# Kernel tuning notes

Hardware: AMD Instinct MI355X
Metric: run time of the kernel (lower is better)

## Reference

```python
import jax, jax.numpy as jnp
import numpy as np

B, M, P = 128, 35, 224  # batch, num Zernike modes, pupil_size
SIGN_PENALTY = 10.0
RECON_WEIGHT = 0.4
DEFOCUS_RAD = 1.0
EPS = 1e-8


def setup_inputs() -> dict:
    key = jax.random.key(0)
    k1, k2, k3, k4 = jax.random.split(key, 4)
    pred = jax.random.normal(k1, (B, M), dtype=jnp.float32)
    target = jax.random.normal(k2, (B, M), dtype=jnp.float32)
    input_psfs = jax.random.uniform(k3, (B, 2, P, P), dtype=jnp.float32)
    zernike_basis = jax.random.normal(k4, (M, P, P), dtype=jnp.float32)
    pupil_mask = jnp.ones((P, P), dtype=jnp.float32)
    return {
        "pred": pred,
        "target": target,
        "input_psfs": input_psfs,
        "zernike_basis": zernike_basis,
        "pupil_mask": pupil_mask,
    }


def _psf_from_phase(phase, pupil_mask):
    # phase: [B,P,P] real; pupil: masked complex field
    pupil = pupil_mask[None, :, :] * jnp.exp(1j * phase)
    field = jnp.fft.fftshift(jnp.fft.fft2(pupil), axes=(-2, -1))
    psf = field.real ** 2 + field.imag ** 2  # |FFT|^2
    psf = psf / (psf.sum(axis=(-2, -1), keepdims=True) + EPS)
    return psf


def reference(pred, target, input_psfs, zernike_basis, pupil_mask):
    # --- sign-weighted MSE on Zernike coefficients ---
    base = (pred - target) ** 2
    sign_match = jnp.sign(pred) * jnp.sign(target)
    weight = jnp.where(sign_match < 0, SIGN_PENALTY, 1.0)
    z_loss = jnp.mean(base * weight)

    # --- batched differentiable PSF reconstruction loss ---
    phase = jnp.einsum('bm,mhw->bhw', pred, zernike_basis)
    phase = phase * pupil_mask[None, :, :]

    sim_if = _psf_from_phase(phase, pupil_mask)  # in-focus

    lin = jnp.linspace(-1.0, 1.0, P, dtype=jnp.float32)
    y, x = jnp.meshgrid(lin, lin, indexing='ij')
    r2 = x ** 2 + y ** 2
    defocus_phase = DEFOCUS_RAD * (2.0 * r2 - 1.0)  # [P,P]
    sim_podf = _psf_from_phase(phase + defocus_phase[None, :, :], pupil_mask)

    # per-sample F.mse_loss then mean over batch == mean over the batched arrays
    recon_loss = (jnp.mean((sim_if - input_psfs[:, 0]) ** 2)
                  + jnp.mean((sim_podf - input_psfs[:, 1]) ** 2))

    return z_loss + RECON_WEIGHT * recon_loss
```

## Files before the change

### kernel.cpp

```cpp
#include <hip/hip_runtime.h>
#include <math.h>

#define BB 128
#define MM 35
#define PSZ 224
#define PP (PSZ*PSZ)
#define SIGN_PENALTY 10.0f
#define RECON_WEIGHT 0.4f
#define DEFOCUS_RAD 1.0f
#define EPS_F 1e-8f
#define INV2PI 0.15915494309189535f


#define WS_PHASE_OFF    2048
#define WS_T_OFF        (WS_PHASE_OFF + BB*PP)
#define N_PARTIALS      (14*BB*2)
#define S1 233
#define S2 20

static constexpr float W16R[16] = {
    1.0f, 0.9238795325f, 0.7071067812f, 0.3826834324f, 0.0f,
    -0.3826834324f, -0.7071067812f, -0.9238795325f, -1.0f,
    -0.9238795325f, -0.7071067812f, -0.3826834324f, 0.0f,
    0.3826834324f, 0.7071067812f, 0.9238795325f};
static constexpr float W16I[16] = {
    0.0f, -0.3826834324f, -0.7071067812f, -0.9238795325f, -1.0f,
    -0.9238795325f, -0.7071067812f, -0.3826834324f, 0.0f,
    0.3826834324f, 0.7071067812f, 0.9238795325f, 1.0f,
    0.9238795325f, 0.7071067812f, 0.3826834324f};
static constexpr float W7R[7] = {
    1.0f, 0.6234898019f, -0.2225209340f, -0.9009688679f,
    -0.9009688679f, -0.2225209340f, 0.6234898019f};
static constexpr float W7I[7] = {
    0.0f, -0.7818314825f, -0.9749279122f, -0.4338837391f,
    0.4338837391f, 0.9749279122f, 0.7818314825f};
static constexpr float W14R[7] = {
    1.0f, 0.9009688679f, 0.6234898019f, 0.2225209340f, -0.2225209340f,
    -0.6234898019f, -0.9009688679f};
static constexpr float W14I[7] = {
    0.0f, -0.4338837391f, -0.7818314825f, -0.9749279122f, -0.9749279122f,
    -0.7818314825f, -0.4338837391f};

__device__ __forceinline__ float lincoord(int i) {
    return -1.0f + 2.0f * (float)i / (float)(PSZ - 1);
}
__device__ __forceinline__ void fast_sincos(float x, float* s, float* c) {
    float rv = x * INV2PI;
    rv -= floorf(rv);
    *s = __builtin_amdgcn_sinf(rv);
    *c = __builtin_amdgcn_cosf(rv);
}
__device__ __forceinline__ float2 wexp_neg(float frac) {
    float rv = -frac;
    rv -= floorf(rv);
    return make_float2(__builtin_amdgcn_cosf(rv), __builtin_amdgcn_sinf(rv));
}
__device__ __forceinline__ unsigned pack_bf2(float a, float b) {
    unsigned r;
    asm("v_cvt_pk_bf16_f32 %0, %1, %2" : "=v"(r) : "v"(a), "v"(b));
    return r;
}
__device__ __forceinline__ float2 unpack_bf2(unsigned v) {
    return make_float2(__uint_as_float(v << 16), __uint_as_float(v & 0xffff0000u));
}
__device__ __forceinline__ float2 cmul(float2 a, float2 b) {
    return make_float2(fmaf(a.x, b.x, -a.y * b.y), fmaf(a.x, b.y, a.y * b.x));
}
__device__ __forceinline__ float2 cmulc(float2 a, float wr, float wi) {
    return make_float2(fmaf(a.x, wr, -a.y * wi), fmaf(a.x, wi, a.y * wr));
}
__device__ __forceinline__ float2 cadd(float2 a, float2 b) {
    return make_float2(a.x + b.x, a.y + b.y);
}
__device__ __forceinline__ float2 csub(float2 a, float2 b) {
    return make_float2(a.x - b.x, a.y - b.y);
}
__device__ __forceinline__ void cfma(float& acc, float c, float v) {
    if (c == 0.f) return;
    if (c == 1.f)  { acc += v; return; }
    if (c == -1.f) { acc -= v; return; }
    acc = fmaf(c, v, acc);
}

__device__ __forceinline__ void dft8_sym(const float2* u, float2* X) {
    float2 a1 = cadd(u[1], u[7]), b1 = csub(u[1], u[7]);
    float2 a2 = cadd(u[2], u[6]), b2 = csub(u[2], u[6]);
    float2 a3 = cadd(u[3], u[5]), b3 = csub(u[3], u[5]);
    float2 s04 = cadd(u[0], u[4]), d04 = csub(u[0], u[4]);
    X[0] = cadd(cadd(s04, a1), cadd(a2, a3));
    X[4] = cadd(csub(s04, a1), csub(a2, a3));
    {
        float2 p = csub(s04, a2);
        float2 q = csub(b1, b3);
        X[2] = make_float2(p.x + q.y, p.y - q.x);
        X[6] = make_float2(p.x - q.y, p.y + q.x);
    }
#pragma unroll
    for (int m = 1; m <= 3; m += 2) {
        float Px = d04.x, Py = d04.y, Qx = 0.f, Qy = 0.f;
#pragma unroll
        for (int n = 1; n <= 3; n++) {
            const float cR = W16R[(2 * n * m) & 15], cI = W16I[(2 * n * m) & 15];
            const float2 a = (n == 1) ? a1 : (n == 2) ? a2 : a3;
            const float2 b = (n == 1) ? b1 : (n == 2) ? b2 : b3;
            cfma(Px, cR, a.x); cfma(Py, cR, a.y);
            cfma(Qx, cI, b.x); cfma(Qy, cI, b.y);
        }
        X[m]     = make_float2(Px - Qy, Py + Qx);
        X[8 - m] = make_float2(Px + Qy, Py - Qx);
    }
}

__device__ __forceinline__ void dft7_sym(const float2* x, float2* X) {
    float2 a1 = cadd(x[1], x[6]), b1 = csub(x[1], x[6]);
    float2 a2 = cadd(x[2], x[5]), b2 = csub(x[2], x[5]);
    float2 a3 = cadd(x[3], x[4]), b3 = csub(x[3], x[4]);
    X[0] = cadd(cadd(x[0], a1), cadd(a2, a3));
#pragma unroll
    for (int k = 1; k <= 3; k++) {
        float Px = x[0].x, Py = x[0].y, Qx = 0.f, Qy = 0.f;
#pragma unroll
        for (int n = 1; n <= 3; n++) {
            const float cR = W7R[(n * k) % 7], cI = W7I[(n * k) % 7];
            const float2 a = (n == 1) ? a1 : (n == 2) ? a2 : a3;
            const float2 b = (n == 1) ? b1 : (n == 2) ? b2 : b3;
            cfma(Px, cR, a.x); cfma(Py, cR, a.y);
            cfma(Qx, cI, b.x); cfma(Qy, cI, b.y);
        }
        X[k]     = make_float2(Px - Qy, Py + Qx);
        X[7 - k] = make_float2(Px + Qy, Py - Qx);
    }
}

__device__ __forceinline__ void inner16_core(const float2* xin,
                                             unsigned* __restrict__ xbuf,
                                             int base, int mul, int n1) {
    float2 u[8], v[8];
#pragma unroll
    for (int n = 0; n < 8; n++) {
        u[n] = cadd(xin[n], xin[n + 8]);
        float2 w = csub(xin[n], xin[n + 8]);
        v[n] = (n == 0) ? w : cmulc(w, W16R[n], W16I[n]);
    }
    float2 u1w = wexp_neg((float)n1 * (1.0f / 224.0f));
    float2 u2w = wexp_neg((float)n1 * (1.0f / 112.0f));
    {
        float2 Xe[8];
        dft8_sym(u, Xe);
        float2 cur = make_float2(1.f, 0.f);
#pragma unroll
        for (int m = 0; m < 8; m++) {
            float2 z = (m == 0) ? Xe[0] : cmul(Xe[m], cur);
            xbuf[base + (14 * (2 * m)) * mul] = pack_bf2(z.x, z.y);
            cur = cmul(cur, u2w);
        }
    }
    {
        float2 Xo[8];
        dft8_sym(v, Xo);
        float2 cur = u1w;
#pragma unroll
        for (int m = 0; m < 8; m++) {
            float2 z = cmul(Xo[m], cur);
            xbuf[base + (14 * (2 * m + 1)) * mul] = pack_bf2(z.x, z.y);
            cur = cmul(cur, u2w);
        }
    }
}

__global__ __launch_bounds__(256) void k_phase(const float* __restrict__ pred,
                                               const float* __restrict__ target,
                                               const float* __restrict__ zern,
                                               const float* __restrict__ mask,
                                               float* __restrict__ phase,
                                               float* __restrict__ ws) {
    __shared__ float pl[32 * MM];
    __shared__ float red[256];
    int t = threadIdx.x;
    if (blockIdx.x == 196) {
        int y = blockIdx.y;
        float s = 0.f;
        if (y == 0) {
            for (int i = t; i < BB * MM; i += 256) {
                float p = pred[i], tg = target[i];
                float dd = p - tg;
                float w = (p * tg < 0.f) ? SIGN_PENALTY : 1.f;
                s = fmaf(dd * dd, w, s);
            }
        } else {
            const int F4 = PP / 4;
            int st = (y - 1) * 4182;
            int en = (y == 3) ? F4 : st + 4182;
            const float4* m4 = (const float4*)mask;
            for (int i = st + t; i < en; i += 256) {
                float4 v = m4[i];
                s = fmaf(v.x, v.x, s); s = fmaf(v.y, v.y, s);
                s = fmaf(v.z, v.z, s); s = fmaf(v.w, v.w, s);
            }
        }
        red[t] = s;
        __syncthreads();
        for (int st = 128; st > 0; st >>= 1) {
            if (t < st) red[t] += red[t + st];
            __syncthreads();
        }
        if (t == 0) {
            if (y == 0) ws[1] = red[0] / (float)(BB * MM);
            else        ws[1 + y] = red[0];
        }
        return;
    }
    int bg = blockIdx.y;
    for (int i = t; i < 32 * MM; i += 256) {
        int j = i / MM, m = i % MM;
        pl[i] = pred[(bg * 32 + j) * MM + m];
    }
    __syncthreads();
    int pix = blockIdx.x * 256 + t;
    float acc[32];
#pragma unroll
    for (int j = 0; j < 32; j++) acc[j] = 0.f;
    for (int m = 0; m < MM; m++) {
        float z = zern[m * PP + pix];
#pragma unroll
        for (int j = 0; j < 32; j++) acc[j] = fmaf(pl[j * MM + m], z, acc[j]);
    }
    float mk = mask[pix];
#pragma unroll
    for (int j = 0; j < 32; j++) phase[(size_t)(bg * 32 + j) * PP + pix] = acc[j] * mk;
}

__global__ __launch_bounds__(256, 5) void k_stage1(const float* __restrict__ phase,
                                                   const float* __restrict__ mask,
                                                   unsigned* __restrict__ T) {
    __shared__ unsigned xs0[16 * S1];
    __shared__ unsigned xs1[16 * S1];
    int h0 = blockIdx.x * 16;
    int b = blockIdx.y;
    int t = threadIdx.x;

    if (t < 224) {
        int r = t / 14, n1 = t - (t / 14) * 14;
        const float* phr = phase + (size_t)b * PP + (size_t)(h0 + r) * PSZ;
        const float* mkr = mask + (size_t)(h0 + r) * PSZ;
        float vy = lincoord(h0 + r);
        float vy2m1 = DEFOCUS_RAD * (2.f * vy * vy - 1.f);
        float2 x0[16];
        unsigned x1p[16];
#pragma unroll
        for (int n = 0; n < 16; n++) {
            int col = n1 + 14 * n;
            float ph = phr[col];
            float mk = mkr[col];
            float sn, cs;
            fast_sincos(ph, &sn, &cs);
            float vx = lincoord(col);
            float df = fmaf(2.f * DEFOCUS_RAD, vx * vx, vy2m1);
            float sd, cd;
            fast_sincos(df, &sd, &cd);
            float c0 = mk * cs, s0 = mk * sn;
            x0[n] = make_float2(c0, s0);
            x1p[n] = pack_bf2(fmaf(c0, cd, -s0 * sd), fmaf(s0, cd, c0 * sd));
        }
        inner16_core(x0, xs0, r * S1 + n1, 1, n1);
        float2 x1[16];
#pragma unroll
        for (int n = 0; n < 16; n++) x1[n] = unpack_bf2(x1p[n]);
        inner16_core(x1, xs1, r * S1 + n1, 1, n1);
    }
    __syncthreads();

    {
        int r = t >> 4, k2 = t & 15;
#pragma unroll
        for (int dd = 0; dd < 2; dd++) {
            const unsigned* xr = (dd ? xs1 : xs0) + r * S1 + k2 * 14;
            int img = dd * BB + b;
            unsigned* Tt = T + (((size_t)img * 14) * PSZ + (h0 + r)) * 16 + k2;
            float2 e[7], E[7], O[7];
#pragma unroll
            for (int n = 0; n < 7; n++) e[n] = unpack_bf2(xr[2 * n]);
            dft7_sym(e, E);
#pragma unroll
            for (int n = 0; n < 7; n++) e[n] = unpack_bf2(xr[2 * n + 1]);
            dft7_sym(e, O);
#pragma unroll
            for (int k1 = 0; k1 < 7; k1++) {
                float2 op = (k1 == 0) ? O[0] : cmulc(O[k1], W14R[k1], W14I[k1]);
                float2 s = cadd(E[k1], op), q = csub(E[k1], op);
                Tt[(size_t)k1 * (PSZ * 16)]       = pack_bf2(s.x, s.y);
                Tt[(size_t)(k1 + 7) * (PSZ * 16)] = pack_bf2(q.x, q.y);
            }
        }
    }
}

__global__ __launch_bounds__(256, 6) void k_stage2(const unsigned* __restrict__ T,
                                                   const float* __restrict__ psfs,
                                                   const float* __restrict__ ws,
                                                   float* __restrict__ partials) {
    __shared__ unsigned xs[224 * S2];
    __shared__ float red[4];
    int tile = blockIdx.x, b = blockIdx.y, d = blockIdx.z;
    int img = d * BB + b;
    int t = threadIdx.x;
    int k2o = t >> 4, c = t & 15;

    const unsigned* Tb = T + ((size_t)img * 14 + tile) * (PSZ * 16);
    const float* inp = psfs + ((size_t)b * 2 + d) * PP;
    int scol = 16 * ((tile + 7) % 14) + c;
    float pf[14];
#pragma unroll
    for (int j = 0; j < 7; j++) {
        pf[j]     = inp[(size_t)(112 + 16 * j + k2o) * PSZ + scol];
        pf[j + 7] = inp[(size_t)(16 * j + k2o) * PSZ + scol];
    }

    if (t < 224) {
        int n1 = t >> 4, cc = t & 15;
        float2 x[16];
#pragma unroll
        for (int n = 0; n < 16; n++)
            x[n] = unpack_bf2(Tb[224 * n + t]);
        inner16_core(x, xs, n1 * S2 + cc, S2, n1);
    }
    __syncthreads();

    float m2 = ws[2] + ws[3] + ws[4];
    float inv_denom = 1.f / (m2 * (float)PP + EPS_F);

    float lsum = 0.f;
    {
        float2 e[7], E[7], O[7];
#pragma unroll
        for (int n = 0; n < 7; n++) e[n] = unpack_bf2(xs[(k2o * 14 + 2 * n) * S2 + c]);
        dft7_sym(e, E);
#pragma unroll
        for (int n = 0; n < 7; n++) e[n] = unpack_bf2(xs[(k2o * 14 + 2 * n + 1) * S2 + c]);
        dft7_sym(e, O);
#pragma unroll
        for (int k1 = 0; k1 < 7; k1++) {
            float2 op = (k1 == 0) ? O[0] : cmulc(O[k1], W14R[k1], W14I[k1]);
            float2 s = cadd(E[k1], op), q = csub(E[k1], op);
            float ds = fmaf(s.x, s.x, s.y * s.y) * inv_denom - pf[k1];
            float dq = fmaf(q.x, q.x, q.y * q.y) * inv_denom - pf[k1 + 7];
            lsum = fmaf(ds, ds, lsum);
            lsum = fmaf(dq, dq, lsum);
        }
    }
#pragma unroll
    for (int off = 32; off > 0; off >>= 1)
        lsum += __shfl_down(lsum, off, 64);
    if ((t & 63) == 0) red[t >> 6] = lsum;
    __syncthreads();
    if (t == 0)
        partials[(blockIdx.z * BB + blockIdx.y) * 14 + blockIdx.x] =
            red[0] + red[1] + red[2] + red[3];
}

__global__ void k_final(const float* __restrict__ ws,
                        const float* __restrict__ partials,
                        float* __restrict__ out) {
    __shared__ float red[256];
    float s = 0.f;
    for (int i = threadIdx.x; i < N_PARTIALS; i += 256) s += partials[i];
    red[threadIdx.x] = s;
    __syncthreads();
    for (int st = 128; st > 0; st >>= 1) {
        if (threadIdx.x < st) red[threadIdx.x] += red[threadIdx.x + st];
        __syncthreads();
    }
    if (threadIdx.x == 0) {
        float recon = red[0] / (float)((size_t)BB * PP);
        out[0] = ws[1] + RECON_WEIGHT * recon;
    }
}

extern "C" void kernel_launch(void* const* d_in, const int* in_sizes, int n_in,
                              void* d_out, int out_size, void* d_ws, size_t ws_size,
                              hipStream_t stream) {
    const float* pred   = (const float*)d_in[0];
    const float* target = (const float*)d_in[1];
    const float* psfs   = (const float*)d_in[2];
    const float* zern   = (const float*)d_in[3];
    const float* mask   = (const float*)d_in[4];

    float*    ws       = (float*)d_ws;
    float*    phase    = ws + WS_PHASE_OFF;
    float*    partials = ws + WS_PHASE_OFF;
    unsigned* T        = (unsigned*)(ws + WS_T_OFF);
    float*    out      = (float*)d_out;

    k_phase<<<dim3(197, 4), 256, 0, stream>>>(pred, target, zern, mask, phase, ws);
    k_stage1<<<dim3(14, BB), 256, 0, stream>>>(phase, mask, T);
    k_stage2<<<dim3(14, BB, 2), 256, 0, stream>>>(T, psfs, ws, partials);
    k_final<<<1, 256, 0, stream>>>(ws, partials, out);
}
```

Baseline: 162.7 us.

## Fuse sincos into phase kernel, store bf16 complex field, vectorize coefficient loads

The phase kernel now computes sin/cos of the phase and writes a packed bf16 complex pupil field instead of fp32 phase. Stage1 reads that field directly and no longer loads the mask or computes the phase sincos. The coefficient tile is padded to 36 so pred values load as float4. Stage2 issues its T loads before the PSF loads, and the occupancy hints are lowered. The aim is less global traffic and fewer transcendental ops; the cost is bf16 rounding of the in-focus field before the FFT and possible occupancy shifts.

```diff
diff --git a/kernel.cpp b/kernel.cpp
--- a/kernel.cpp
+++ b/kernel.cpp
@@ -172,9 +172,9 @@
                                                const float* __restrict__ target,
                                                const float* __restrict__ zern,
                                                const float* __restrict__ mask,
-                                               float* __restrict__ phase,
+                                               unsigned* __restrict__ field,
                                                float* __restrict__ ws) {
-    __shared__ float pl[32 * MM];
+    __shared__ __align__(16) float pl[32 * 36];
     __shared__ float red[256];
     int t = threadIdx.x;
     if (blockIdx.x == 196) {
@@ -212,26 +212,53 @@
     }
     int bg = blockIdx.y;
     for (int i = t; i < 32 * MM; i += 256) {
-        int j = i / MM, m = i % MM;
-        pl[i] = pred[(bg * 32 + j) * MM + m];
-    }
+        int j = i / MM, m = i - (i / MM) * MM;
+        pl[j * 36 + m] = pred[(bg * 32 + j) * MM + m];
+    }
+    if (t < 32) pl[t * 36 + 35] = 0.f;
     __syncthreads();
     int pix = blockIdx.x * 256 + t;
     float acc[32];
 #pragma unroll
     for (int j = 0; j < 32; j++) acc[j] = 0.f;
-    for (int m = 0; m < MM; m++) {
-        float z = zern[m * PP + pix];
-#pragma unroll
-        for (int j = 0; j < 32; j++) acc[j] = fmaf(pl[j * MM + m], z, acc[j]);
+    const float4* pl4 = (const float4*)pl;
+    for (int mb = 0; mb < 32; mb += 4) {
+        float z0 = zern[(size_t)(mb + 0) * PP + pix];
+        float z1 = zern[(size_t)(mb + 1) * PP + pix];
+        float z2 = zern[(size_t)(mb + 2) * PP + pix];
+        float z3 = zern[(size_t)(mb + 3) * PP + pix];
+#pragma unroll
+        for (int j = 0; j < 32; j++) {
+            float4 p4 = pl4[j * 9 + (mb >> 2)];
+            acc[j] = fmaf(p4.x, z0, acc[j]);
+            acc[j] = fmaf(p4.y, z1, acc[j]);
+            acc[j] = fmaf(p4.z, z2, acc[j]);
+            acc[j] = fmaf(p4.w, z3, acc[j]);
+        }
+    }
+    {
+        float z0 = zern[(size_t)32 * PP + pix];
+        float z1 = zern[(size_t)33 * PP + pix];
+        float z2 = zern[(size_t)34 * PP + pix];
+#pragma unroll
+        for (int j = 0; j < 32; j++) {
+            float4 p4 = pl4[j * 9 + 8];
+            acc[j] = fmaf(p4.x, z0, acc[j]);
+            acc[j] = fmaf(p4.y, z1, acc[j]);
+            acc[j] = fmaf(p4.z, z2, acc[j]);
+        }
     }
     float mk = mask[pix];
 #pragma unroll
-    for (int j = 0; j < 32; j++) phase[(size_t)(bg * 32 + j) * PP + pix] = acc[j] * mk;
-}
-
-__global__ __launch_bounds__(256, 5) void k_stage1(const float* __restrict__ phase,
-                                                   const float* __restrict__ mask,
+    for (int j = 0; j < 32; j++) {
+        float ph = acc[j] * mk;
+        float sn, cs;
+        fast_sincos(ph, &sn, &cs);
+        field[(size_t)(bg * 32 + j) * PP + pix] = pack_bf2(mk * cs, mk * sn);
+    }
+}
+
+__global__ __launch_bounds__(256, 4) void k_stage1(const unsigned* __restrict__ field,
                                                    unsigned* __restrict__ T) {
     __shared__ unsigned xs0[16 * S1];
     __shared__ unsigned xs1[16 * S1];
@@ -241,8 +268,7 @@
 
     if (t < 224) {
         int r = t / 14, n1 = t - (t / 14) * 14;
-        const float* phr = phase + (size_t)b * PP + (size_t)(h0 + r) * PSZ;
-        const float* mkr = mask + (size_t)(h0 + r) * PSZ;
+        const unsigned* fr = field + (size_t)b * PP + (size_t)(h0 + r) * PSZ;
         float vy = lincoord(h0 + r);
         float vy2m1 = DEFOCUS_RAD * (2.f * vy * vy - 1.f);
         float2 x0[16];
@@ -250,17 +276,13 @@
 #pragma unroll
         for (int n = 0; n < 16; n++) {
             int col = n1 + 14 * n;
-            float ph = phr[col];
-            float mk = mkr[col];
-            float sn, cs;
-            fast_sincos(ph, &sn, &cs);
+            float2 f = unpack_bf2(fr[col]);
             float vx = lincoord(col);
             float df = fmaf(2.f * DEFOCUS_RAD, vx * vx, vy2m1);
             float sd, cd;
             fast_sincos(df, &sd, &cd);
-            float c0 = mk * cs, s0 = mk * sn;
-            x0[n] = make_float2(c0, s0);
-            x1p[n] = pack_bf2(fmaf(c0, cd, -s0 * sd), fmaf(s0, cd, c0 * sd));
+            x0[n] = f;
+            x1p[n] = pack_bf2(fmaf(f.x, cd, -f.y * sd), fmaf(f.y, cd, f.x * sd));
         }
         inner16_core(x0, xs0, r * S1 + n1, 1, n1);
         float2 x1[16];
@@ -295,7 +317,7 @@
     }
 }
 
-__global__ __launch_bounds__(256, 6) void k_stage2(const unsigned* __restrict__ T,
+__global__ __launch_bounds__(256, 5) void k_stage2(const unsigned* __restrict__ T,
                                                    const float* __restrict__ psfs,
                                                    const float* __restrict__ ws,
                                                    float* __restrict__ partials) {
@@ -305,10 +327,17 @@
     int img = d * BB + b;
     int t = threadIdx.x;
     int k2o = t >> 4, c = t & 15;
+    bool act = t < 224;
 
     const unsigned* Tb = T + ((size_t)img * 14 + tile) * (PSZ * 16);
     const float* inp = psfs + ((size_t)b * 2 + d) * PP;
     int scol = 16 * ((tile + 7) % 14) + c;
+
+    unsigned xr[16];
+    if (act) {
+#pragma unroll
+        for (int n = 0; n < 16; n++) xr[n] = Tb[224 * n + t];
+    }
     float pf[14];
 #pragma unroll
     for (int j = 0; j < 7; j++) {
@@ -316,13 +345,11 @@
         pf[j + 7] = inp[(size_t)(16 * j + k2o) * PSZ + scol];
     }
 
-    if (t < 224) {
-        int n1 = t >> 4, cc = t & 15;
+    if (act) {
         float2 x[16];
 #pragma unroll
-        for (int n = 0; n < 16; n++)
-            x[n] = unpack_bf2(Tb[224 * n + t]);
-        inner16_core(x, xs, n1 * S2 + cc, S2, n1);
+        for (int n = 0; n < 16; n++) x[n] = unpack_bf2(xr[n]);
+        inner16_core(x, xs, (t >> 4) * S2 + (t & 15), S2, t >> 4);
     }
     __syncthreads();
 
@@ -386,13 +413,13 @@
     const float* mask   = (const float*)d_in[4];
 
     float*    ws       = (float*)d_ws;
-    float*    phase    = ws + WS_PHASE_OFF;
+    unsigned* field    = (unsigned*)(ws + WS_PHASE_OFF);
     float*    partials = ws + WS_PHASE_OFF;
     unsigned* T        = (unsigned*)(ws + WS_T_OFF);
     float*    out      = (float*)d_out;
 
-    k_phase<<<dim3(197, 4), 256, 0, stream>>>(pred, target, zern, mask, phase, ws);
-    k_stage1<<<dim3(14, BB), 256, 0, stream>>>(phase, mask, T);
+    k_phase<<<dim3(197, 4), 256, 0, stream>>>(pred, target, zern, mask, field, ws);
+    k_stage1<<<dim3(14, BB), 256, 0, stream>>>(field, T);
     k_stage2<<<dim3(14, BB, 2), 256, 0, stream>>>(T, psfs, ws, partials);
     k_final<<<1, 256, 0, stream>>>(ws, partials, out);
 }
```

Result: faster. 154.6 us (-5.0%).
